# Kernel tuning notes

Measured on AMD Instinct MI355X. Metric: run time of the kernel, lower is better.

Reference implementation:

```python
import jax, jax.numpy as jnp
import numpy as np

N_NODES = 50000
IN_CH = 128
HID = 32
HEADS = 4
OUT_CH = 32
N_EDGES = 1600000
NEG_SLOPE = 0.2


def _gatv2(x, src, dst, Wl, bl, Wr, br, att, bias, H, C):
    """GATv2Conv (PyG semantics, add_self_loops already applied to src/dst).
    x: [N, F_in]; src/dst: [E]; Wl/Wr: [F_in, H*C]; att: [H, C]; bias: [H*C].
    Returns [N, H*C] (concat heads)."""
    N = x.shape[0]
    xl = (x @ Wl + bl).reshape(N, H, C)  # source-side transform
    xr = (x @ Wr + br).reshape(N, H, C)  # target-side transform
    e = jax.nn.leaky_relu(xl[src] + xr[dst], NEG_SLOPE)  # [E, H, C]
    logits = jnp.einsum('ehc,hc->eh', e, att)  # [E, H]
    # softmax over incoming edges of each target node (stable)
    m = jax.ops.segment_max(logits, dst, num_segments=N)[dst]
    p = jnp.exp(logits - m)
    denom = jax.ops.segment_sum(p, dst, num_segments=N)[dst]
    alpha = p / denom  # [E, H]
    out = jax.ops.segment_sum(alpha[:, :, None] * xl[src], dst, num_segments=N)
    return out.reshape(N, H * C) + bias


def setup_inputs() -> dict:
    key = jax.random.key(0)
    ks = jax.random.split(key, 16)
    s1 = 1.0 / np.sqrt(IN_CH)
    s2 = 1.0 / np.sqrt(HID * HEADS)
    inp = {
        'x': jax.random.normal(ks[0], (N_NODES, IN_CH), jnp.float32),
        'edge_index': jax.random.randint(ks[1], (2, N_EDGES), 0, N_NODES, jnp.int64 if jax.config.read('jax_enable_x64') else jnp.int32).astype(jnp.int32),
        # layer 1: in -> HID per head, HEADS heads
        'Wl1': jax.random.normal(ks[2], (IN_CH, HEADS * HID), jnp.float32) * s1,
        'bl1': jnp.zeros((HEADS * HID,), jnp.float32),
        'Wr1': jax.random.normal(ks[3], (IN_CH, HEADS * HID), jnp.float32) * s1,
        'br1': jnp.zeros((HEADS * HID,), jnp.float32),
        'att1': jax.random.normal(ks[4], (HEADS, HID), jnp.float32) * s1,
        'b1': jnp.zeros((HEADS * HID,), jnp.float32),
        # mu head: HID*HEADS -> OUT_CH, 1 head
        'Wl_mu': jax.random.normal(ks[5], (HEADS * HID, OUT_CH), jnp.float32) * s2,
        'bl_mu': jnp.zeros((OUT_CH,), jnp.float32),
        'Wr_mu': jax.random.normal(ks[6], (HEADS * HID, OUT_CH), jnp.float32) * s2,
        'br_mu': jnp.zeros((OUT_CH,), jnp.float32),
        'att_mu': jax.random.normal(ks[7], (1, OUT_CH), jnp.float32) * s2,
        'b_mu': jnp.zeros((OUT_CH,), jnp.float32),
        # logvar head
        'Wl_lv': jax.random.normal(ks[8], (HEADS * HID, OUT_CH), jnp.float32) * s2,
        'bl_lv': jnp.zeros((OUT_CH,), jnp.float32),
        'Wr_lv': jax.random.normal(ks[9], (HEADS * HID, OUT_CH), jnp.float32) * s2,
        'br_lv': jnp.zeros((OUT_CH,), jnp.float32),
        'att_lv': jax.random.normal(ks[10], (1, OUT_CH), jnp.float32) * s2,
        'b_lv': jnp.zeros((OUT_CH,), jnp.float32),
    }
    return inp


def reference(x, edge_index, Wl1, bl1, Wr1, br1, att1, b1,
              Wl_mu, bl_mu, Wr_mu, br_mu, att_mu, b_mu,
              Wl_lv, bl_lv, Wr_lv, br_lv, att_lv, b_lv):
    N = x.shape[0]
    loops = jnp.arange(N, dtype=edge_index.dtype)
    src = jnp.concatenate([edge_index[0], loops])  # add_self_loops=True
    dst = jnp.concatenate([edge_index[1], loops])
    h = jax.nn.relu(_gatv2(x, src, dst, Wl1, bl1, Wr1, br1, att1, b1, HEADS, HID))
    mu = _gatv2(h, src, dst, Wl_mu, bl_mu, Wr_mu, br_mu, att_mu, b_mu, 1, OUT_CH)
    logvar = _gatv2(h, src, dst, Wl_lv, bl_lv, Wr_lv, br_lv, att_lv, b_lv, 1, OUT_CH)
    return (mu, logvar)
```

## Files before the change

kernel.cpp:

```cpp
#include <hip/hip_runtime.h>
#include <hip/hip_fp16.h>

#define NNODES 50000
#define EORIG  1600000
#define ETOT   (EORIG + NNODES)
#define NEG 0.2f
#define BSH 7
#define NBUCK ((NNODES + 127) >> BSH)
#define NRT (NNODES / 16)

typedef _Float16 v2h __attribute__((ext_vector_type(2)));
typedef _Float16 v8h __attribute__((ext_vector_type(8)));
typedef float    v4f __attribute__((ext_vector_type(4)));

__device__ __forceinline__ float hdot2v(v2h a, v2h b, float c) {
#if __has_builtin(__builtin_amdgcn_fdot2)
    return __builtin_amdgcn_fdot2(a, b, c, false);
#else
    return c + (float)a.x * (float)b.x + (float)a.y * (float)b.y;
#endif
}

__global__ __launch_bounds__(256) void wcvt_kernel(
    const float* __restrict__ Wl, const float* __restrict__ Wr,
    const float* __restrict__ Wlmu, const float* __restrict__ Wllv,
    const float* __restrict__ Wrmu, const float* __restrict__ Wrlv,
    __half* __restrict__ WT, __half* __restrict__ WT2)
{
    int id = blockIdx.x * 256 + threadIdx.x;
    if (id < 32768) {
        int k = id >> 8, c = id & 255;
        float v = (c < 128) ? Wl[k * 128 + c] : Wr[k * 128 + (c - 128)];
        WT[c * 128 + k] = __float2half(v);
    } else if (id < 49152) {
        int loc = id - 32768;
        int k = loc >> 7, c = loc & 127;
        int sel = c >> 5, cc = c & 31;
        const float* W = sel == 0 ? Wlmu : sel == 1 ? Wllv : sel == 2 ? Wrmu : Wrlv;
        WT2[c * 128 + k] = __float2half(W[k * 32 + cc]);
    }
}

__global__ __launch_bounds__(256) void lin1_kernel(
    const float* __restrict__ x, const __half* __restrict__ WT,
    const float* __restrict__ bl, const float* __restrict__ br,
    __half* __restrict__ xl16, __half* __restrict__ xr16)
{
    int rt = (blockIdx.x * 256 + threadIdx.x) >> 6;
    if (rt >= NRT) return;
    int l  = threadIdx.x & 63;
    int lr = l & 15, lg = l >> 4;
    int row = rt * 16 + lr;

    v8h a[4];
    const float4* xrow = reinterpret_cast<const float4*>(x + (size_t)row * 128);
    #pragma unroll
    for (int ks = 0; ks < 4; ++ks) {
        float4 f0 = xrow[ks * 8 + lg * 2];
        float4 f1 = xrow[ks * 8 + lg * 2 + 1];
        v8h t;
        t[0]=(_Float16)f0.x; t[1]=(_Float16)f0.y; t[2]=(_Float16)f0.z; t[3]=(_Float16)f0.w;
        t[4]=(_Float16)f1.x; t[5]=(_Float16)f1.y; t[6]=(_Float16)f1.z; t[7]=(_Float16)f1.w;
        a[ks] = t;
    }

    const uint4* wt4 = reinterpret_cast<const uint4*>(WT);
    #pragma unroll 4
    for (int ct = 0; ct < 16; ++ct) {
        int c = ct * 16 + lr;
        v4f acc = {0.f, 0.f, 0.f, 0.f};
        #pragma unroll
        for (int ks = 0; ks < 4; ++ks) {
            union { uint4 u; v8h h; } B;
            B.u = wt4[(size_t)c * 16 + ks * 4 + lg];
            acc = __builtin_amdgcn_mfma_f32_16x16x32_f16(a[ks], B.h, acc, 0, 0, 0);
        }
        float bb = (c < 128) ? bl[c] : br[c - 128];
        #pragma unroll
        for (int j = 0; j < 4; ++j) {
            int orow = rt * 16 + lg * 4 + j;
            __half hv = __float2half(acc[j] + bb);
            if (c < 128) xl16[(size_t)orow * 128 + c] = hv;
            else         xr16[(size_t)orow * 128 + (c - 128)] = hv;
        }
    }
}

__global__ __launch_bounds__(256) void lin2_kernel(
    const __half* __restrict__ h16, const __half* __restrict__ WT2,
    const float* __restrict__ blmu, const float* __restrict__ bllv,
    const float* __restrict__ brmu, const float* __restrict__ brlv,
    __half* __restrict__ xi16, __half* __restrict__ xrI16)
{
    int rt = (blockIdx.x * 256 + threadIdx.x) >> 6;
    if (rt >= NRT) return;
    int l  = threadIdx.x & 63;
    int lr = l & 15, lg = l >> 4;
    int row = rt * 16 + lr;

    v8h a[4];
    const uint4* hrow = reinterpret_cast<const uint4*>(h16 + (size_t)row * 128);
    #pragma unroll
    for (int ks = 0; ks < 4; ++ks) {
        union { uint4 u; v8h h; } A;
        A.u = hrow[ks * 4 + lg];
        a[ks] = A.h;
    }

    const uint4* wt4 = reinterpret_cast<const uint4*>(WT2);
    #pragma unroll 4
    for (int ct = 0; ct < 8; ++ct) {
        int c = ct * 16 + lr;
        v4f acc = {0.f, 0.f, 0.f, 0.f};
        #pragma unroll
        for (int ks = 0; ks < 4; ++ks) {
            union { uint4 u; v8h h; } B;
            B.u = wt4[(size_t)c * 16 + ks * 4 + lg];
            acc = __builtin_amdgcn_mfma_f32_16x16x32_f16(a[ks], B.h, acc, 0, 0, 0);
        }
        int sel = c >> 5, cc = c & 31;
        const float* bp = sel == 0 ? blmu : sel == 1 ? bllv : sel == 2 ? brmu : brlv;
        float bb = bp[cc];
        #pragma unroll
        for (int j = 0; j < 4; ++j) {
            int orow = rt * 16 + lg * 4 + j;
            __half hv = __float2half(acc[j] + bb);
            if (c < 64) xi16 [(size_t)orow * 64 + c]      = hv;
            else        xrI16[(size_t)orow * 64 + (c-64)] = hv;
        }
    }
}

__global__ __launch_bounds__(256) void bhist_kernel(
    const int* __restrict__ dst, int* __restrict__ btot)
{
    __shared__ int cnt[NBUCK];
    for (int i = threadIdx.x; i < NBUCK; i += 256) cnt[i] = 0;
    __syncthreads();
    const int e0 = blockIdx.x * 8192;
    for (int i = threadIdx.x; i < 8192; i += 256) {
        int e = e0 + i;
        if (e >= ETOT) break;
        int d = (e < EORIG) ? dst[e] : e - EORIG;
        atomicAdd(&cnt[d >> BSH], 1);
    }
    __syncthreads();
    for (int i = threadIdx.x; i < NBUCK; i += 256)
        if (cnt[i]) atomicAdd(&btot[i], cnt[i]);
}

__global__ __launch_bounds__(512) void bscan_kernel(
    const int* __restrict__ btot, int* __restrict__ bbase, int* __restrict__ bcur)
{
    __shared__ int tmp[512];
    int t = threadIdx.x;
    int v = (t < NBUCK) ? btot[t] : 0;
    tmp[t] = v;
    __syncthreads();
    for (int off = 1; off < 512; off <<= 1) {
        int a = (t >= off) ? tmp[t - off] : 0;
        __syncthreads();
        tmp[t] += a;
        __syncthreads();
    }
    if (t < NBUCK) { int e = tmp[t] - v; bbase[t] = e; bcur[t] = e; }
    if (t == 0) bbase[NBUCK] = ETOT;
}

__global__ __launch_bounds__(256) void part_kernel(
    const int* __restrict__ src, const int* __restrict__ dst,
    int* __restrict__ bcur, int2* __restrict__ pairs)
{
    __shared__ int cnt[NBUCK];
    __shared__ int gbase[NBUCK];
    const int e0 = blockIdx.x * 8192;

    for (int i = threadIdx.x; i < NBUCK; i += 256) cnt[i] = 0;
    __syncthreads();

    for (int i = threadIdx.x; i < 8192; i += 256) {
        int e = e0 + i;
        if (e >= ETOT) break;
        int d = (e < EORIG) ? dst[e] : e - EORIG;
        atomicAdd(&cnt[d >> BSH], 1);
    }
    __syncthreads();

    for (int b = threadIdx.x; b < NBUCK; b += 256) {
        int c = cnt[b];
        gbase[b] = c ? atomicAdd(&bcur[b], c) : 0;
        cnt[b] = 0;
    }
    __syncthreads();

    for (int i = threadIdx.x; i < 8192; i += 256) {
        int e = e0 + i;
        if (e >= ETOT) break;
        int s, d;
        if (e < EORIG) { s = src[e]; d = dst[e]; }
        else           { s = d = e - EORIG; }
        int b = d >> BSH;
        int slot = atomicAdd(&cnt[b], 1);
        pairs[gbase[b] + slot] = make_int2(s, d);
    }
}

__global__ __launch_bounds__(256) void csrfill_kernel(
    const int2* __restrict__ pairs, const int* __restrict__ bbase,
    int* __restrict__ offs, int* __restrict__ csr)
{
    __shared__ int cnt[128];
    __shared__ int lofs[128];
    __shared__ int scnt[128];
    const int b = blockIdx.x, n0 = b << BSH;
    const int nn = min(128, NNODES - n0);
    const int pbeg = bbase[b], pend = bbase[b + 1];
    const int t = threadIdx.x;

    if (t < 128) { cnt[t] = 0; scnt[t] = 0; }
    __syncthreads();
    for (int i = pbeg + t; i < pend; i += 256)
        atomicAdd(&cnt[pairs[i].y - n0], 1);
    __syncthreads();

    if (t < 128) lofs[t] = cnt[t];
    __syncthreads();
    for (int off = 1; off < 128; off <<= 1) {
        int v = (t < 128 && t >= off) ? lofs[t - off] : 0;
        __syncthreads();
        if (t < 128) lofs[t] += v;
        __syncthreads();
    }
    if (t < 128) lofs[t] = pbeg + lofs[t] - cnt[t];
    __syncthreads();

    if (t < nn) offs[n0 + t] = lofs[t];
    if (b == NBUCK - 1 && t == 0) offs[NNODES] = ETOT;

    for (int i = pbeg + t; i < pend; i += 256) {
        int2 pr = pairs[i];
        int l = pr.y - n0;
        int slot = atomicAdd(&scnt[l], 1);
        csr[lofs[l] + slot] = pr.x;
    }
}

__global__ __launch_bounds__(256) void gat_gather1(
    const __half* __restrict__ xl16, const __half* __restrict__ xr16,
    const float* __restrict__ att, const float* __restrict__ bias,
    const int* __restrict__ offs, const int* __restrict__ csr,
    __half* __restrict__ h16)
{
    int d = (blockIdx.x * 256 + threadIdx.x) >> 6;
    if (d >= NNODES) return;
    int lane = threadIdx.x & 63;
    int quarter = lane >> 4;
    int q = lane & 15;

    v2h xrh[4], ath[4];
    {
        union { uint4 u; v2h v[4]; } R;
        R.u = reinterpret_cast<const uint4*>(xr16)[(size_t)d * 16 + q];
        #pragma unroll
        for (int j = 0; j < 4; ++j) xrh[j] = R.v[j];
        const float4* t4 = reinterpret_cast<const float4*>(att) + q * 2;
        float4 a = t4[0], b = t4[1];
        ath[0] = (v2h){(_Float16)a.x, (_Float16)a.y};
        ath[1] = (v2h){(_Float16)a.z, (_Float16)a.w};
        ath[2] = (v2h){(_Float16)b.x, (_Float16)b.y};
        ath[3] = (v2h){(_Float16)b.z, (_Float16)b.w};
    }
    const v2h neg2 = (v2h){(_Float16)NEG, (_Float16)NEG};

    int beg = offs[d], end = offs[d + 1];
    float den = 0.f;
    float acc[8] = {0.f,0.f,0.f,0.f,0.f,0.f,0.f,0.f};
    const uint4* xlu = reinterpret_cast<const uint4*>(xl16);

    for (int base = beg; base < end; base += 8) {
        int si[2]; bool val[2];
        #pragma unroll
        for (int k = 0; k < 2; ++k) {
            int sl = base + quarter * 2 + k;
            val[k] = sl < end;
            si[k]  = csr[val[k] ? sl : end - 1];
        }
        uint4 xv[2];
        #pragma unroll
        for (int k = 0; k < 2; ++k)
            xv[k] = xlu[(size_t)si[k] * 16 + q];
        #pragma unroll
        for (int k = 0; k < 2; ++k) {
            union { uint4 u; v2h v[4]; } U; U.u = xv[k];
            float t = 0.f;
            #pragma unroll
            for (int j = 0; j < 4; ++j) {
                v2h s = U.v[j] + xrh[j];
                v2h l = __builtin_elementwise_max(s, s * neg2);
                t = hdot2v(l, ath[j], t);
            }
            t += __shfl_xor(t, 1, 64);
            t += __shfl_xor(t, 2, 64);
            float p = val[k] ? __expf(t) : 0.f;
            den += p;
            #pragma unroll
            for (int j = 0; j < 4; ++j) {
                acc[2*j]   += p * (float)U.v[j].x;
                acc[2*j+1] += p * (float)U.v[j].y;
            }
        }
    }

    den += __shfl_xor(den, 16, 64);
    den += __shfl_xor(den, 32, 64);
    #pragma unroll
    for (int j = 0; j < 8; ++j) {
        acc[j] += __shfl_xor(acc[j], 16, 64);
        acc[j] += __shfl_xor(acc[j], 32, 64);
    }

    if (quarter == 0) {
        float r = 1.f / den;
        const float4* bp = reinterpret_cast<const float4*>(bias) + q * 2;
        float4 ba = bp[0], bb = bp[1];
        __half hv[8];
        hv[0] = __float2half(fmaxf(acc[0]*r+ba.x, 0.f));
        hv[1] = __float2half(fmaxf(acc[1]*r+ba.y, 0.f));
        hv[2] = __float2half(fmaxf(acc[2]*r+ba.z, 0.f));
        hv[3] = __float2half(fmaxf(acc[3]*r+ba.w, 0.f));
        hv[4] = __float2half(fmaxf(acc[4]*r+bb.x, 0.f));
        hv[5] = __float2half(fmaxf(acc[5]*r+bb.y, 0.f));
        hv[6] = __float2half(fmaxf(acc[6]*r+bb.z, 0.f));
        hv[7] = __float2half(fmaxf(acc[7]*r+bb.w, 0.f));
        *reinterpret_cast<uint4*>(&h16[(size_t)d * 128 + q * 8]) =
            *reinterpret_cast<uint4*>(hv);
    }
}

__global__ __launch_bounds__(256) void gat_gather2(
    const __half* __restrict__ xi16, const __half* __restrict__ xrI16,
    const float* __restrict__ atmu, const float* __restrict__ atlv,
    const float* __restrict__ bmu,  const float* __restrict__ blv,
    const int* __restrict__ offs, const int* __restrict__ csr,
    float* __restrict__ out)
{
    int d = (blockIdx.x * 256 + threadIdx.x) >> 6;
    if (d >= NNODES) return;
    int lane = threadIdx.x & 63;
    int oct = lane >> 3;
    int r   = lane & 7;
    bool lv = r >= 4;
    int cq  = lv ? r - 4 : r;

    v2h xrh[4], ath[4];
    {
        union { uint4 u; v2h v[4]; } R;
        R.u = reinterpret_cast<const uint4*>(xrI16)[(size_t)d * 8 + r];
        #pragma unroll
        for (int j = 0; j < 4; ++j) xrh[j] = R.v[j];
        const float4* t4 = reinterpret_cast<const float4*>(lv ? atlv : atmu) + cq * 2;
        float4 a = t4[0], b = t4[1];
        ath[0] = (v2h){(_Float16)a.x, (_Float16)a.y};
        ath[1] = (v2h){(_Float16)a.z, (_Float16)a.w};
        ath[2] = (v2h){(_Float16)b.x, (_Float16)b.y};
        ath[3] = (v2h){(_Float16)b.z, (_Float16)b.w};
    }
    const v2h neg2 = (v2h){(_Float16)NEG, (_Float16)NEG};

    int beg = offs[d], end = offs[d + 1];
    float den = 0.f;
    float acc[8] = {0.f,0.f,0.f,0.f,0.f,0.f,0.f,0.f};
    const uint4* xiu = reinterpret_cast<const uint4*>(xi16);

    for (int base = beg; base < end; base += 16) {
        int si[2]; bool val[2];
        #pragma unroll
        for (int k = 0; k < 2; ++k) {
            int sl = base + oct * 2 + k;
            val[k] = sl < end;
            si[k]  = csr[val[k] ? sl : end - 1];
        }
        uint4 xv[2];
        #pragma unroll
        for (int k = 0; k < 2; ++k)
            xv[k] = xiu[(size_t)si[k] * 8 + r];
        #pragma unroll
        for (int k = 0; k < 2; ++k) {
            union { uint4 u; v2h v[4]; } U; U.u = xv[k];
            float t = 0.f;
            #pragma unroll
            for (int j = 0; j < 4; ++j) {
                v2h s = U.v[j] + xrh[j];
                v2h l = __builtin_elementwise_max(s, s * neg2);
                t = hdot2v(l, ath[j], t);
            }
            t += __shfl_xor(t, 1, 64);
            t += __shfl_xor(t, 2, 64);
            float p = val[k] ? __expf(t) : 0.f;
            den += p;
            #pragma unroll
            for (int j = 0; j < 4; ++j) {
                acc[2*j]   += p * (float)U.v[j].x;
                acc[2*j+1] += p * (float)U.v[j].y;
            }
        }
    }

    den += __shfl_xor(den, 8, 64);
    den += __shfl_xor(den, 16, 64);
    den += __shfl_xor(den, 32, 64);
    #pragma unroll
    for (int j = 0; j < 8; ++j) {
        acc[j] += __shfl_xor(acc[j], 8, 64);
        acc[j] += __shfl_xor(acc[j], 16, 64);
        acc[j] += __shfl_xor(acc[j], 32, 64);
    }

    if (oct == 0) {
        float rr = 1.f / den;
        const float4* bp = reinterpret_cast<const float4*>(lv ? blv : bmu) + cq * 2;
        float4 ba = bp[0], bb = bp[1];
        float4 o1 = make_float4(acc[0]*rr+ba.x, acc[1]*rr+ba.y,
                                acc[2]*rr+ba.z, acc[3]*rr+ba.w);
        float4 o2 = make_float4(acc[4]*rr+bb.x, acc[5]*rr+bb.y,
                                acc[6]*rr+bb.z, acc[7]*rr+bb.w);
        float* base_out = out + (lv ? 1600000 : 0);
        float4* op = reinterpret_cast<float4*>(base_out) + (size_t)d * 8 + cq * 2;
        op[0] = o1; op[1] = o2;
    }
}

extern "C" void kernel_launch(void* const* d_in, const int* in_sizes, int n_in,
                              void* d_out, int out_size, void* d_ws, size_t ws_size,
                              hipStream_t stream) {
    const float* x    = (const float*)d_in[0];
    const int*   ei   = (const int*)d_in[1];
    const float* Wl1  = (const float*)d_in[2];
    const float* bl1  = (const float*)d_in[3];
    const float* Wr1  = (const float*)d_in[4];
    const float* br1  = (const float*)d_in[5];
    const float* att1 = (const float*)d_in[6];
    const float* b1   = (const float*)d_in[7];
    const float* Wlmu = (const float*)d_in[8];
    const float* blmu = (const float*)d_in[9];
    const float* Wrmu = (const float*)d_in[10];
    const float* brmu = (const float*)d_in[11];
    const float* atmu = (const float*)d_in[12];
    const float* bmu  = (const float*)d_in[13];
    const float* Wllv = (const float*)d_in[14];
    const float* bllv = (const float*)d_in[15];
    const float* Wrlv = (const float*)d_in[16];
    const float* brlv = (const float*)d_in[17];
    const float* atlv = (const float*)d_in[18];
    const float* blv  = (const float*)d_in[19];

    float* out = (float*)d_out;
    float* ws  = (float*)d_ws;

    __half* xl16 = (__half*)ws;
    __half* xr16 = (__half*)(ws + 3200000);
    __half* h16  = (__half*)(ws + 6400000);
    __half* WT   = (__half*)(ws + 9600000);
    __half* WT2  = (__half*)(ws + 9620000);

    __half* xi16  = (__half*)ws;
    __half* xrI16 = (__half*)(ws + 1600000);

    int*  ip    = (int*)(ws + 10000000);
    int2* pairs = (int2*)ip;
    int*  btot  = ip + 3300000;
    int*  bbase = ip + 3300400;
    int*  bcur  = ip + 3300800;
    int*  offs  = ip + 3301200;
    int*  csr   = ip + 3351204;

    const int* srcp = ei;
    const int* dstp = ei + EORIG;

    const int NBE = (ETOT + 8191) / 8192;

    wcvt_kernel<<<192, 256, 0, stream>>>(Wl1, Wr1, Wlmu, Wllv, Wrmu, Wrlv, WT, WT2);

    hipMemsetAsync(btot, 0, NBUCK * sizeof(int), stream);
    bhist_kernel<<<NBE, 256, 0, stream>>>(dstp, btot);
    bscan_kernel<<<1, 512, 0, stream>>>(btot, bbase, bcur);
    part_kernel<<<NBE, 256, 0, stream>>>(srcp, dstp, bcur, pairs);
    csrfill_kernel<<<NBUCK, 256, 0, stream>>>(pairs, bbase, offs, csr);

    lin1_kernel<<<(NRT + 3) / 4, 256, 0, stream>>>(x, WT, bl1, br1, xl16, xr16);

    gat_gather1<<<(NNODES * 64 + 255) / 256, 256, 0, stream>>>(
        xl16, xr16, att1, b1, offs, csr, h16);

    lin2_kernel<<<(NRT + 3) / 4, 256, 0, stream>>>(
        h16, WT2, blmu, bllv, brmu, brlv, xi16, xrI16);

    gat_gather2<<<(NNODES * 64 + 255) / 256, 256, 0, stream>>>(
        xi16, xrI16, atmu, atlv, bmu, blv, offs, csr, out);
}
```

Baseline: 221.0 us.

## Compress CSR to 16-bit indices, software-pipeline gathers, fold memset into weight convert

Edge pairs are packed into one 32-bit word (16-bit source plus 7-bit local destination) and the CSR column array becomes 16-bit, which cuts partition and gather index traffic. Both gather kernels get a software pipeline that prefetches indices two steps ahead and feature rows one step ahead, to hide dependent load latency. The btot memset is folded into wcvt_kernel, and edges per partition block drop to 4096 for more blocks. The 16-bit source index only holds values up to 65535, which works for 50000 nodes but is not general, and the prefetch adds register pressure.

```diff
diff --git a/kernel.cpp b/kernel.cpp
--- a/kernel.cpp
+++ b/kernel.cpp
@@ -8,6 +8,7 @@
 #define BSH 7
 #define NBUCK ((NNODES + 127) >> BSH)
 #define NRT (NNODES / 16)
+#define EPB 4096
 
 typedef _Float16 v2h __attribute__((ext_vector_type(2)));
 typedef _Float16 v8h __attribute__((ext_vector_type(8)));
@@ -25,9 +26,10 @@
     const float* __restrict__ Wl, const float* __restrict__ Wr,
     const float* __restrict__ Wlmu, const float* __restrict__ Wllv,
     const float* __restrict__ Wrmu, const float* __restrict__ Wrlv,
-    __half* __restrict__ WT, __half* __restrict__ WT2)
+    __half* __restrict__ WT, __half* __restrict__ WT2, int* __restrict__ btot)
 {
     int id = blockIdx.x * 256 + threadIdx.x;
+    if (id < NBUCK) btot[id] = 0;
     if (id < 32768) {
         int k = id >> 8, c = id & 255;
         float v = (c < 128) ? Wl[k * 128 + c] : Wr[k * 128 + (c - 128)];
@@ -137,8 +139,8 @@
     __shared__ int cnt[NBUCK];
     for (int i = threadIdx.x; i < NBUCK; i += 256) cnt[i] = 0;
     __syncthreads();
-    const int e0 = blockIdx.x * 8192;
-    for (int i = threadIdx.x; i < 8192; i += 256) {
+    const int e0 = blockIdx.x * EPB;
+    for (int i = threadIdx.x; i < EPB; i += 256) {
         int e = e0 + i;
         if (e >= ETOT) break;
         int d = (e < EORIG) ? dst[e] : e - EORIG;
@@ -169,16 +171,16 @@
 
 __global__ __launch_bounds__(256) void part_kernel(
     const int* __restrict__ src, const int* __restrict__ dst,
-    int* __restrict__ bcur, int2* __restrict__ pairs)
+    int* __restrict__ bcur, unsigned int* __restrict__ pairs)
 {
     __shared__ int cnt[NBUCK];
     __shared__ int gbase[NBUCK];
-    const int e0 = blockIdx.x * 8192;
+    const int e0 = blockIdx.x * EPB;
 
     for (int i = threadIdx.x; i < NBUCK; i += 256) cnt[i] = 0;
     __syncthreads();
 
-    for (int i = threadIdx.x; i < 8192; i += 256) {
+    for (int i = threadIdx.x; i < EPB; i += 256) {
         int e = e0 + i;
         if (e >= ETOT) break;
         int d = (e < EORIG) ? dst[e] : e - EORIG;
@@ -193,7 +195,7 @@
     }
     __syncthreads();
 
-    for (int i = threadIdx.x; i < 8192; i += 256) {
+    for (int i = threadIdx.x; i < EPB; i += 256) {
         int e = e0 + i;
         if (e >= ETOT) break;
         int s, d;
@@ -201,13 +203,13 @@
         else           { s = d = e - EORIG; }
         int b = d >> BSH;
         int slot = atomicAdd(&cnt[b], 1);
-        pairs[gbase[b] + slot] = make_int2(s, d);
+        pairs[gbase[b] + slot] = (unsigned)s | ((unsigned)(d & 127) << 16);
     }
 }
 
 __global__ __launch_bounds__(256) void csrfill_kernel(
-    const int2* __restrict__ pairs, const int* __restrict__ bbase,
-    int* __restrict__ offs, int* __restrict__ csr)
+    const unsigned int* __restrict__ pairs, const int* __restrict__ bbase,
+    int* __restrict__ offs, unsigned short* __restrict__ csr)
 {
     __shared__ int cnt[128];
     __shared__ int lofs[128];
@@ -220,7 +222,7 @@
     if (t < 128) { cnt[t] = 0; scnt[t] = 0; }
     __syncthreads();
     for (int i = pbeg + t; i < pend; i += 256)
-        atomicAdd(&cnt[pairs[i].y - n0], 1);
+        atomicAdd(&cnt[pairs[i] >> 16], 1);
     __syncthreads();
 
     if (t < 128) lofs[t] = cnt[t];
@@ -238,17 +240,17 @@
     if (b == NBUCK - 1 && t == 0) offs[NNODES] = ETOT;
 
     for (int i = pbeg + t; i < pend; i += 256) {
-        int2 pr = pairs[i];
-        int l = pr.y - n0;
+        unsigned pr = pairs[i];
+        int l = pr >> 16;
         int slot = atomicAdd(&scnt[l], 1);
-        csr[lofs[l] + slot] = pr.x;
+        csr[lofs[l] + slot] = (unsigned short)(pr & 0xFFFFu);
     }
 }
 
 __global__ __launch_bounds__(256) void gat_gather1(
     const __half* __restrict__ xl16, const __half* __restrict__ xr16,
     const float* __restrict__ att, const float* __restrict__ bias,
-    const int* __restrict__ offs, const int* __restrict__ csr,
+    const int* __restrict__ offs, const unsigned short* __restrict__ csr,
     __half* __restrict__ h16)
 {
     int d = (blockIdx.x * 256 + threadIdx.x) >> 6;
@@ -256,6 +258,7 @@
     int lane = threadIdx.x & 63;
     int quarter = lane >> 4;
     int q = lane & 15;
+    int off0 = quarter * 2, off1 = off0 + 1;
 
     v2h xrh[4], ath[4];
     {
@@ -273,42 +276,56 @@
     const v2h neg2 = (v2h){(_Float16)NEG, (_Float16)NEG};
 
     int beg = offs[d], end = offs[d + 1];
+    int nI = (end - beg + 7) >> 3;
+    const uint4* xlu = reinterpret_cast<const uint4*>(xl16);
+
     float den = 0.f;
     float acc[8] = {0.f,0.f,0.f,0.f,0.f,0.f,0.f,0.f};
-    const uint4* xlu = reinterpret_cast<const uint4*>(xl16);
-
-    for (int base = beg; base < end; base += 8) {
-        int si[2]; bool val[2];
-        #pragma unroll
-        for (int k = 0; k < 2; ++k) {
-            int sl = base + quarter * 2 + k;
-            val[k] = sl < end;
-            si[k]  = csr[val[k] ? sl : end - 1];
-        }
-        uint4 xv[2];
-        #pragma unroll
-        for (int k = 0; k < 2; ++k)
-            xv[k] = xlu[(size_t)si[k] * 16 + q];
-        #pragma unroll
-        for (int k = 0; k < 2; ++k) {
-            union { uint4 u; v2h v[4]; } U; U.u = xv[k];
-            float t = 0.f;
-            #pragma unroll
-            for (int j = 0; j < 4; ++j) {
-                v2h s = U.v[j] + xrh[j];
-                v2h l = __builtin_elementwise_max(s, s * neg2);
-                t = hdot2v(l, ath[j], t);
-            }
-            t += __shfl_xor(t, 1, 64);
-            t += __shfl_xor(t, 2, 64);
-            float p = val[k] ? __expf(t) : 0.f;
-            den += p;
-            #pragma unroll
-            for (int j = 0; j < 4; ++j) {
-                acc[2*j]   += p * (float)U.v[j].x;
-                acc[2*j+1] += p * (float)U.v[j].y;
-            }
-        }
+
+    auto compute = [&](uint4 U, bool val) {
+        union { uint4 u; v2h v[4]; } X; X.u = U;
+        float t = 0.f;
+        #pragma unroll
+        for (int j = 0; j < 4; ++j) {
+            v2h s = X.v[j] + xrh[j];
+            v2h l = __builtin_elementwise_max(s, s * neg2);
+            t = hdot2v(l, ath[j], t);
+        }
+        t += __shfl_xor(t, 1, 64);
+        t += __shfl_xor(t, 2, 64);
+        float p = val ? __expf(t) : 0.f;
+        den += p;
+        #pragma unroll
+        for (int j = 0; j < 4; ++j) {
+            acc[2*j]   += p * (float)X.v[j].x;
+            acc[2*j+1] += p * (float)X.v[j].y;
+        }
+    };
+
+    int sA0 = beg + off0, sA1 = beg + off1;
+    bool vA0 = sA0 < end, vA1 = sA1 < end;
+    int iA0 = csr[vA0 ? sA0 : end - 1];
+    int iA1 = csr[vA1 ? sA1 : end - 1];
+    uint4 rA0 = xlu[(size_t)iA0 * 16 + q];
+    uint4 rA1 = xlu[(size_t)iA1 * 16 + q];
+
+    int sB0 = beg + 8 + off0, sB1 = beg + 8 + off1;
+    bool vB0 = sB0 < end, vB1 = sB1 < end;
+    int iB0 = csr[vB0 ? sB0 : end - 1];
+    int iB1 = csr[vB1 ? sB1 : end - 1];
+
+    for (int it = 0; it < nI; ++it) {
+        int b2 = beg + (it + 2) * 8;
+        int sC0 = b2 + off0, sC1 = b2 + off1;
+        bool vC0 = sC0 < end, vC1 = sC1 < end;
+        int iC0 = csr[vC0 ? sC0 : end - 1];
+        int iC1 = csr[vC1 ? sC1 : end - 1];
+        uint4 rB0 = xlu[(size_t)iB0 * 16 + q];
+        uint4 rB1 = xlu[(size_t)iB1 * 16 + q];
+        compute(rA0, vA0);
+        compute(rA1, vA1);
+        rA0 = rB0; rA1 = rB1; vA0 = vB0; vA1 = vB1;
+        iB0 = iC0; iB1 = iC1; vB0 = vC0; vB1 = vC1;
     }
 
     den += __shfl_xor(den, 16, 64);
@@ -341,7 +358,7 @@
     const __half* __restrict__ xi16, const __half* __restrict__ xrI16,
     const float* __restrict__ atmu, const float* __restrict__ atlv,
     const float* __restrict__ bmu,  const float* __restrict__ blv,
-    const int* __restrict__ offs, const int* __restrict__ csr,
+    const int* __restrict__ offs, const unsigned short* __restrict__ csr,
     float* __restrict__ out)
 {
     int d = (blockIdx.x * 256 + threadIdx.x) >> 6;
@@ -351,6 +368,7 @@
     int r   = lane & 7;
     bool lv = r >= 4;
     int cq  = lv ? r - 4 : r;
+    int off0 = oct * 2, off1 = off0 + 1;
 
     v2h xrh[4], ath[4];
     {
@@ -368,42 +386,56 @@
     const v2h neg2 = (v2h){(_Float16)NEG, (_Float16)NEG};
 
     int beg = offs[d], end = offs[d + 1];
+    int nI = (end - beg + 15) >> 4;
+    const uint4* xiu = reinterpret_cast<const uint4*>(xi16);
+
     float den = 0.f;
     float acc[8] = {0.f,0.f,0.f,0.f,0.f,0.f,0.f,0.f};
-    const uint4* xiu = reinterpret_cast<const uint4*>(xi16);
-
-    for (int base = beg; base < end; base += 16) {
-        int si[2]; bool val[2];
-        #pragma unroll
-        for (int k = 0; k < 2; ++k) {
-            int sl = base + oct * 2 + k;
-            val[k] = sl < end;
-            si[k]  = csr[val[k] ? sl : end - 1];
-        }
-        uint4 xv[2];
-        #pragma unroll
-        for (int k = 0; k < 2; ++k)
-            xv[k] = xiu[(size_t)si[k] * 8 + r];
-        #pragma unroll
-        for (int k = 0; k < 2; ++k) {
-            union { uint4 u; v2h v[4]; } U; U.u = xv[k];
-            float t = 0.f;
-            #pragma unroll
-            for (int j = 0; j < 4; ++j) {
-                v2h s = U.v[j] + xrh[j];
-                v2h l = __builtin_elementwise_max(s, s * neg2);
-                t = hdot2v(l, ath[j], t);
-            }
-            t += __shfl_xor(t, 1, 64);
-            t += __shfl_xor(t, 2, 64);
-            float p = val[k] ? __expf(t) : 0.f;
-            den += p;
-            #pragma unroll
-            for (int j = 0; j < 4; ++j) {
-                acc[2*j]   += p * (float)U.v[j].x;
-                acc[2*j+1] += p * (float)U.v[j].y;
-            }
-        }
+
+    auto compute = [&](uint4 U, bool val) {
+        union { uint4 u; v2h v[4]; } X; X.u = U;
+        float t = 0.f;
+        #pragma unroll
+        for (int j = 0; j < 4; ++j) {
+            v2h s = X.v[j] + xrh[j];
+            v2h l = __builtin_elementwise_max(s, s * neg2);
+            t = hdot2v(l, ath[j], t);
+        }
+        t += __shfl_xor(t, 1, 64);
+        t += __shfl_xor(t, 2, 64);
+        float p = val ? __expf(t) : 0.f;
+        den += p;
+        #pragma unroll
+        for (int j = 0; j < 4; ++j) {
+            acc[2*j]   += p * (float)X.v[j].x;
+            acc[2*j+1] += p * (float)X.v[j].y;
+        }
+    };
+
+    int sA0 = beg + off0, sA1 = beg + off1;
+    bool vA0 = sA0 < end, vA1 = sA1 < end;
+    int iA0 = csr[vA0 ? sA0 : end - 1];
+    int iA1 = csr[vA1 ? sA1 : end - 1];
+    uint4 rA0 = xiu[(size_t)iA0 * 8 + r];
+    uint4 rA1 = xiu[(size_t)iA1 * 8 + r];
+
+    int sB0 = beg + 16 + off0, sB1 = beg + 16 + off1;
+    bool vB0 = sB0 < end, vB1 = sB1 < end;
+    int iB0 = csr[vB0 ? sB0 : end - 1];
+    int iB1 = csr[vB1 ? sB1 : end - 1];
+
+    for (int it = 0; it < nI; ++it) {
+        int b2 = beg + (it + 2) * 16;
+        int sC0 = b2 + off0, sC1 = b2 + off1;
+        bool vC0 = sC0 < end, vC1 = sC1 < end;
+        int iC0 = csr[vC0 ? sC0 : end - 1];
+        int iC1 = csr[vC1 ? sC1 : end - 1];
+        uint4 rB0 = xiu[(size_t)iB0 * 8 + r];
+        uint4 rB1 = xiu[(size_t)iB1 * 8 + r];
+        compute(rA0, vA0);
+        compute(rA1, vA1);
+        rA0 = rB0; rA1 = rB1; vA0 = vB0; vA1 = vB1;
+        iB0 = iC0; iB1 = iC1; vB0 = vC0; vB1 = vC1;
     }
 
     den += __shfl_xor(den, 8, 64);
@@ -466,22 +498,21 @@
     __half* xi16  = (__half*)ws;
     __half* xrI16 = (__half*)(ws + 1600000);
 
-    int*  ip    = (int*)(ws + 10000000);
-    int2* pairs = (int2*)ip;
-    int*  btot  = ip + 3300000;
-    int*  bbase = ip + 3300400;
-    int*  bcur  = ip + 3300800;
-    int*  offs  = ip + 3301200;
-    int*  csr   = ip + 3351204;
+    int* ip = (int*)(ws + 10000000);
+    unsigned int*   pairs = (unsigned int*)ip;
+    int*            btot  = ip + 1650000;
+    int*            bbase = ip + 1650400;
+    int*            bcur  = ip + 1650800;
+    int*            offs  = ip + 1651200;
+    unsigned short* csr   = (unsigned short*)(ip + 1701204);
 
     const int* srcp = ei;
     const int* dstp = ei + EORIG;
 
-    const int NBE = (ETOT + 8191) / 8192;
-
-    wcvt_kernel<<<192, 256, 0, stream>>>(Wl1, Wr1, Wlmu, Wllv, Wrmu, Wrlv, WT, WT2);
-
-    hipMemsetAsync(btot, 0, NBUCK * sizeof(int), stream);
+    const int NBE = (ETOT + EPB - 1) / EPB;
+
+    wcvt_kernel<<<192, 256, 0, stream>>>(Wl1, Wr1, Wlmu, Wllv, Wrmu, Wrlv, WT, WT2, btot);
+
     bhist_kernel<<<NBE, 256, 0, stream>>>(dstp, btot);
     bscan_kernel<<<1, 512, 0, stream>>>(btot, bbase, bcur);
     part_kernel<<<NBE, 256, 0, stream>>>(srcp, dstp, bcur, pairs);
```

Result: faster. 210.3 us (-4.9%).
